# Performance work log

Measured on AMD Instinct MI355X. Metric: run time of the kernel, lower is better.

Reference implementation:

```python
import jax, jax.numpy as jnp
import numpy as np

NEG_SLOPE = 0.2   # PyG GATConv default negative_slope
BN_EPS = 1e-5


def gat_layer(x, src, dst, W, a_src, a_dst, b, num_nodes):
    """PyG-style GATConv (concat=True). src/dst already include self-loops."""
    H, C = a_src.shape
    h = (x @ W).reshape(num_nodes, H, C)            # [N,H,C]
    al_s = jnp.sum(h * a_src, axis=-1)              # [N,H] per-node src score
    al_d = jnp.sum(h * a_dst, axis=-1)              # [N,H]
    e = al_s[src] + al_d[dst]                       # [E,H]
    e = jnp.where(e > 0, e, NEG_SLOPE * e)          # leaky_relu
    m = jax.ops.segment_max(e, dst, num_segments=num_nodes)
    e = jnp.exp(e - m[dst])
    s = jax.ops.segment_sum(e, dst, num_segments=num_nodes)
    alpha = e / (s[dst] + 1e-16)                    # segment softmax over dst
    out = jax.ops.segment_sum(alpha[:, :, None] * h[src], dst, num_segments=num_nodes)
    return out.reshape(num_nodes, H * C) + b


def batch_norm(x, gamma, beta):
    mu = jnp.mean(x, axis=0)
    var = jnp.mean((x - mu) ** 2, axis=0)
    return (x - mu) * jax.lax.rsqrt(var + BN_EPS) * gamma + beta


def setup_inputs() -> dict:
    N, E, IN, H, C, L, OUT, NC = 50000, 800000, 256, 4, 64, 32, 32, 30
    HC = H * C
    key = jax.random.key(0)
    cnt = [0]
    def nk():
        cnt[0] += 1
        return jax.random.fold_in(key, cnt[0])
    def w(shape, scale):
        return jax.random.normal(nk(), shape, jnp.float32) * scale
    inp = {
        "x": jax.random.normal(nk(), (N, IN), jnp.float32),
        "edge_index": jax.random.randint(nk(), (2, E), 0, N, dtype=jnp.int32),
        "eps": jax.random.normal(nk(), (N, L), jnp.float32),
    }
    for i, d_in in zip((1, 2, 3), (IN, HC, HC)):
        inp[f"W{i}"] = w((d_in, HC), 1.0 / np.sqrt(d_in))
        inp[f"asrc{i}"] = w((H, C), 0.1)
        inp[f"adst{i}"] = w((H, C), 0.1)
        inp[f"b{i}"] = jnp.zeros((HC,), jnp.float32)
        inp[f"g{i}"] = jnp.ones((HC,), jnp.float32)
        inp[f"be{i}"] = jnp.zeros((HC,), jnp.float32)
    inp["Wr"] = w((IN, HC), 1.0 / np.sqrt(IN)); inp["br"] = jnp.zeros((HC,), jnp.float32)
    inp["Wmu"] = w((HC, L), 1.0 / np.sqrt(HC)); inp["bmu"] = jnp.zeros((L,), jnp.float32)
    inp["Wlv"] = w((HC, L), 1.0 / np.sqrt(HC)); inp["blv"] = jnp.zeros((L,), jnp.float32)
    inp["Wd"] = w((L, OUT), 1.0 / np.sqrt(L)); inp["bd"] = jnp.zeros((OUT,), jnp.float32)
    inp["Wa"] = w((HC, NC), 1.0 / np.sqrt(HC)); inp["ba"] = jnp.zeros((NC,), jnp.float32)
    return inp


def reference(x, edge_index, eps,
              W1, asrc1, adst1, b1, g1, be1,
              W2, asrc2, adst2, b2, g2, be2,
              W3, asrc3, adst3, b3, g3, be3,
              Wr, br, Wmu, bmu, Wlv, blv, Wd, bd, Wa, ba):
    N = x.shape[0]
    loop = jnp.arange(N, dtype=edge_index.dtype)   # PyG add_self_loops default
    src = jnp.concatenate([edge_index[0], loop])
    dst = jnp.concatenate([edge_index[1], loop])

    residual = x @ Wr + br                          # [N, HC]
    h = jax.nn.relu(batch_norm(gat_layer(x, src, dst, W1, asrc1, adst1, b1, N), g1, be1))
    h = jax.nn.relu(batch_norm(gat_layer(h, src, dst, W2, asrc2, adst2, b2, N), g2, be2))
    h = jax.nn.relu(batch_norm(gat_layer(h, src, dst, W3, asrc3, adst3, b3, N), g3, be3))
    enc = h + residual

    mu = enc @ Wmu + bmu
    logvar = enc @ Wlv + blv
    z = mu + eps * jnp.exp(0.5 * logvar)            # reparameterize
    out = z @ Wd + bd
    aux_out = enc @ Wa + ba
    return (out, mu, logvar, aux_out, enc)
```

## Files before the change

kernel.cpp:

```cpp
#include <hip/hip_runtime.h>
#include <cstdint>

typedef __bf16 bf16;
typedef float f32x4 __attribute__((ext_vector_type(4)));
typedef _Float16 fp16;
typedef _Float16 half8 __attribute__((ext_vector_type(8)));

#define NEG_SLOPE 0.2f
#define BN_EPS 1e-5f

__device__ __forceinline__ void gld_lds16(const void* g, void* l) {
  auto gp = reinterpret_cast<const __attribute__((address_space(1))) unsigned int*>(
      reinterpret_cast<uintptr_t>(g));
  auto lp = reinterpret_cast<__attribute__((address_space(3))) unsigned int*>(
      reinterpret_cast<uintptr_t>(l));
  __builtin_amdgcn_global_load_lds(gp, lp, 16, 0, 0);
}

__global__ __launch_bounds__(256) void k_prep(
    const float* __restrict__ Wr, const float* __restrict__ W1,
    const float* __restrict__ W2, const float* __restrict__ W3,
    fp16* __restrict__ Wt0, fp16* __restrict__ Wt1,
    fp16* __restrict__ Wt2, fp16* __restrict__ Wt3,
    const float* __restrict__ Wmu, const float* __restrict__ bmu,
    const float* __restrict__ Wlv, const float* __restrict__ blv,
    const float* __restrict__ Wa, const float* __restrict__ ba,
    fp16* __restrict__ Wh, float* __restrict__ bias_cat,
    const float* __restrict__ x, fp16* __restrict__ A16,
    int* __restrict__ counts, int N, int xb) {
  const int b = blockIdx.x, t = threadIdx.x;
  if (b < 1024) {
    const int m = b >> 8, k = b & 255;
    const float* W = (m == 0) ? Wr : (m == 1) ? W1 : (m == 2) ? W2 : W3;
    fp16* Wt = (m == 0) ? Wt0 : (m == 1) ? Wt1 : (m == 2) ? Wt2 : Wt3;
    Wt[t * 256 + k] = (fp16)W[k * 256 + t];
  } else if (b < 1280) {
    const int k = b - 1024;
    if (t < 128) {
      float v = 0.f;
      if (t < 32) v = Wmu[k * 32 + t];
      else if (t < 64) v = Wlv[k * 32 + (t - 32)];
      else if (t < 94) v = Wa[k * 30 + (t - 64)];
      Wh[t * 256 + k] = (fp16)v;
      if (k == 0) {
        float bb = 0.f;
        if (t < 32) bb = bmu[t];
        else if (t < 64) bb = blv[t - 32];
        else if (t < 94) bb = ba[t - 64];
        bias_cat[t] = bb;
      }
    }
  } else if (b < 1280 + xb) {
    const size_t base = (size_t)(b - 1280) * 1024 + t;
    const size_t total = (size_t)N * 256;
#pragma unroll
    for (int r = 0; r < 4; ++r) {
      size_t i = base + (size_t)r * 256;
      if (i < total) A16[i] = (fp16)x[i];
    }
  } else {
    const int i = (b - 1280 - xb) * 256 + t;
    if (i < N) counts[i] = 1;
  }
}

__global__ void k_count(const int* __restrict__ ei, int* counts, int E) {
  int i = blockIdx.x * 256 + threadIdx.x;
  if (i < E) atomicAdd(&counts[ei[E + i]], 1);
}

__global__ __launch_bounds__(256) void k_scan1(const int* __restrict__ counts,
                                               int* __restrict__ row_start,
                                               int* __restrict__ bsums, int N) {
  __shared__ int s[256];
  const int t = threadIdx.x;
  const int idx = blockIdx.x * 1024 + t * 4;
  int a0 = (idx + 0 < N) ? counts[idx + 0] : 0;
  int a1 = (idx + 1 < N) ? counts[idx + 1] : 0;
  int a2 = (idx + 2 < N) ? counts[idx + 2] : 0;
  int a3 = (idx + 3 < N) ? counts[idx + 3] : 0;
  const int mysum = a0 + a1 + a2 + a3;
  s[t] = mysum;
  __syncthreads();
  for (int ofs = 1; ofs < 256; ofs <<= 1) {
    int v = (t >= ofs) ? s[t - ofs] : 0;
    __syncthreads();
    s[t] += v;
    __syncthreads();
  }
  int excl = s[t] - mysum;
  if (idx + 0 < N) row_start[idx + 0] = excl;
  if (idx + 1 < N) row_start[idx + 1] = excl + a0;
  if (idx + 2 < N) row_start[idx + 2] = excl + a0 + a1;
  if (idx + 3 < N) row_start[idx + 3] = excl + a0 + a1 + a2;
  if (t == 255) bsums[blockIdx.x] = s[255];
}

__global__ void k_scan2(int* __restrict__ bsums, int* __restrict__ row_start, int nb, int N) {
  if (threadIdx.x == 0 && blockIdx.x == 0) {
    int run = 0;
    for (int i = 0; i < nb; ++i) {
      int v = bsums[i];
      bsums[i] = run;
      run += v;
    }
    row_start[N] = run;
  }
}

__global__ void k_scan3(int* __restrict__ row_start, int* __restrict__ cursor,
                        const int* __restrict__ bsums, int N) {
  int i = blockIdx.x * 256 + threadIdx.x;
  if (i < N) {
    int v = row_start[i] + bsums[i >> 10];
    row_start[i] = v;
    cursor[i] = v;
  }
}

__global__ void k_fill(const int* __restrict__ ei, int* cursor, int* __restrict__ csr_src,
                       int E, int N) {
  int i = blockIdx.x * 256 + threadIdx.x;
  if (i < E) {
    int s = ei[i], d = ei[E + i];
    int p = atomicAdd(&cursor[d], 1);
    csr_src[p] = s;
  } else if (i < E + N) {
    int n = i - E;
    int p = atomicAdd(&cursor[n], 1);
    csr_src[p] = n;
  }
}

__global__ __launch_bounds__(256) void k_gemm(
    const fp16* __restrict__ A16, const fp16* __restrict__ B16,
    const float* __restrict__ bias, float* __restrict__ Cf, fp16* __restrict__ C16,
    const float* __restrict__ asrcp, const float* __restrict__ adstp,
    float* __restrict__ alsp, float* __restrict__ aldp,
    int M, int ldc) {
  __shared__ fp16 Ash[128 * 32];
  __shared__ fp16 Bsh[128 * 32];
  const int t = threadIdx.x;
  const int wave = t >> 6, lane = t & 63;
  const int m0 = blockIdx.x * 128, n0 = blockIdx.y * 128;
  const int lrow = lane & 15, lq = lane >> 4;
  const int wm = (wave >> 1) * 64, wn = (wave & 1) * 64;

  f32x4 acc[4][4] = {};

  const int j0 = wave * 64 + lane, j1 = j0 + 256;
  const int ar0 = j0 >> 2, ar1 = j1 >> 2;
  const int ak0 = ((j0 & 3) ^ ((ar0 >> 1) & 3)) * 8;
  const int ak1 = ((j1 & 3) ^ ((ar1 >> 1) & 3)) * 8;
  const int gm0 = min(m0 + ar0, M - 1), gm1 = min(m0 + ar1, M - 1);
  const size_t oa0 = (size_t)gm0 * 256 + ak0, oa1 = (size_t)gm1 * 256 + ak1;
  const size_t ob0 = (size_t)(n0 + ar0) * 256 + ak0, ob1 = (size_t)(n0 + ar1) * 256 + ak1;
  const int l0 = wave * 512, l1 = 2048 + wave * 512;

  for (int k0 = 0; k0 < 256; k0 += 32) {
    __syncthreads();
    gld_lds16(A16 + oa0 + k0, Ash + l0);
    gld_lds16(A16 + oa1 + k0, Ash + l1);
    gld_lds16(B16 + ob0 + k0, Bsh + l0);
    gld_lds16(B16 + ob1 + k0, Bsh + l1);
    __syncthreads();
    half8 af[4], bf[4];
#pragma unroll
    for (int mi = 0; mi < 4; mi++) {
      int row = wm + mi * 16 + lrow;
      int off = row * 32 + ((lq ^ ((row >> 1) & 3)) << 3);
      af[mi] = *(const half8*)(Ash + off);
    }
#pragma unroll
    for (int ni = 0; ni < 4; ni++) {
      int row = wn + ni * 16 + lrow;
      int off = row * 32 + ((lq ^ ((row >> 1) & 3)) << 3);
      bf[ni] = *(const half8*)(Bsh + off);
    }
#pragma unroll
    for (int mi = 0; mi < 4; mi++)
#pragma unroll
      for (int ni = 0; ni < 4; ni++)
        acc[mi][ni] = __builtin_amdgcn_mfma_f32_16x16x32_f16(af[mi], bf[ni], acc[mi][ni], 0, 0, 0);
  }

#pragma unroll
  for (int mi = 0; mi < 4; mi++) {
    const int mb = m0 + wm + mi * 16 + lq * 4;
#pragma unroll
    for (int ni = 0; ni < 4; ni++) {
      const int n = n0 + wn + ni * 16 + lrow;
#pragma unroll
      for (int r = 0; r < 4; r++) {
        int m = mb + r;
        if (m < M) {
          if (C16) C16[(size_t)m * ldc + n] = (fp16)acc[mi][ni][r];
          else     Cf[(size_t)m * ldc + n] = acc[mi][ni][r] + (bias ? bias[n] : 0.f);
        }
      }
    }
  }

  if (asrcp) {
    const int headg = (n0 + wn) >> 6;
    float as4[4], ad4[4];
#pragma unroll
    for (int ni = 0; ni < 4; ni++) {
      int cg = n0 + wn + ni * 16 + lrow;
      as4[ni] = asrcp[cg];
      ad4[ni] = adstp[cg];
    }
#pragma unroll
    for (int mi = 0; mi < 4; mi++) {
      float ps[4] = {0.f, 0.f, 0.f, 0.f}, pd[4] = {0.f, 0.f, 0.f, 0.f};
#pragma unroll
      for (int ni = 0; ni < 4; ni++)
#pragma unroll
        for (int r = 0; r < 4; r++) {
          ps[r] += acc[mi][ni][r] * as4[ni];
          pd[r] += acc[mi][ni][r] * ad4[ni];
        }
#pragma unroll
      for (int o = 1; o < 16; o <<= 1)
#pragma unroll
        for (int r = 0; r < 4; r++) {
          ps[r] += __shfl_xor(ps[r], o, 64);
          pd[r] += __shfl_xor(pd[r], o, 64);
        }
      if (lrow == 0) {
#pragma unroll
        for (int r = 0; r < 4; r++) {
          int m = m0 + wm + mi * 16 + lq * 4 + r;
          if (m < M) {
            alsp[(size_t)m * 4 + headg] = ps[r];
            aldp[(size_t)m * 4 + headg] = pd[r];
          }
        }
      }
    }
  }
}

__global__ __launch_bounds__(256) void k_gather(
    const fp16* __restrict__ h16, const float* __restrict__ als, const float* __restrict__ ald,
    const int* __restrict__ row_start, const int* __restrict__ csr_src,
    const float* __restrict__ bias, fp16* __restrict__ out, float* __restrict__ stats, int N) {
  if (blockIdx.x == 0) { stats[threadIdx.x] = 0.f; stats[256 + threadIdx.x] = 0.f; }
  const int wave = threadIdx.x >> 6, lane = threadIdx.x & 63;
  const int half = lane >> 5, l32 = lane & 31;
  const int n = blockIdx.x * 8 + wave * 2 + half;
  if (n >= N) return;
  const int head = l32 >> 3;
  const int c0 = l32 * 8;
  const float adh = ald[(size_t)n * 4 + head];
  const int beg = row_start[n], end = row_start[n + 1];
  float s = 0.f;
  float acc[8] = {0.f, 0.f, 0.f, 0.f, 0.f, 0.f, 0.f, 0.f};
#pragma unroll 4
  for (int i = beg; i < end; ++i) {
    const int sidx = csr_src[i];
    float e = als[(size_t)sidx * 4 + head] + adh;
    e = e > 0.f ? e : NEG_SLOPE * e;
    const float w = __expf(e);
    s += w;
    const half8 hv = *(const half8*)(h16 + (size_t)sidx * 256 + c0);
#pragma unroll
    for (int k = 0; k < 8; ++k) acc[k] += w * (float)hv[k];
  }
  const float inv = 1.f / (s + 1e-16f);
  const float4 b1 = *(const float4*)(bias + c0);
  const float4 b2 = *(const float4*)(bias + c0 + 4);
  half8 o;
  o[0] = (fp16)(acc[0] * inv + b1.x); o[1] = (fp16)(acc[1] * inv + b1.y);
  o[2] = (fp16)(acc[2] * inv + b1.z); o[3] = (fp16)(acc[3] * inv + b1.w);
  o[4] = (fp16)(acc[4] * inv + b2.x); o[5] = (fp16)(acc[5] * inv + b2.y);
  o[6] = (fp16)(acc[6] * inv + b2.z); o[7] = (fp16)(acc[7] * inv + b2.w);
  *(half8*)(out + (size_t)n * 256 + c0) = o;
}

__global__ __launch_bounds__(256) void k_bn_stats(const fp16* __restrict__ x,
                                                  float* __restrict__ stats, int N) {
  const int t = threadIdx.x;
  int r0 = blockIdx.x * 128;
  int rend = min(r0 + 128, N);
  float s = 0.f, sq = 0.f;
  for (int r = r0; r < rend; ++r) {
    float v = (float)x[(size_t)r * 256 + t];
    s += v; sq += v * v;
  }
  atomicAdd(&stats[t], s);
  atomicAdd(&stats[256 + t], sq);
}

__global__ __launch_bounds__(256) void k_bn_apply(
    const fp16* __restrict__ x, const float* __restrict__ stats,
    const float* __restrict__ g, const float* __restrict__ be,
    fp16* __restrict__ act16, float* __restrict__ encf,
    float invN, int total) {
  int idx = blockIdx.x * 256 + threadIdx.x;
  if (idx >= total) return;
  int c = idx & 255;
  float mu = stats[c] * invN;
  float var = stats[256 + c] * invN - mu * mu;
  float v = ((float)x[idx] - mu) * rsqrtf(var + BN_EPS) * g[c] + be[c];
  v = fmaxf(v, 0.f);
  if (encf) { v += encf[idx]; encf[idx] = v; }
  act16[idx] = (fp16)v;
}

__global__ __launch_bounds__(256) void k_finish(
    const float* __restrict__ HEAD, const float* __restrict__ eps,
    const float* __restrict__ Wd, const float* __restrict__ bd,
    float* __restrict__ o_out, float* __restrict__ o_mu, float* __restrict__ o_lv,
    float* __restrict__ o_aux, int N) {
  __shared__ float sWd[1024];
  __shared__ float sZ[8][33];
  const int t = threadIdx.x;
  for (int i = t; i < 1024; i += 256) sWd[i] = Wd[i];
  __syncthreads();
  const int r = t >> 5, j = t & 31;
  const int n = blockIdx.x * 8 + r;
  if (n < N) {
    const float* hp = HEAD + (size_t)n * 128;
    float mu = hp[j];
    float lv = hp[32 + j];
    float z = mu + eps[(size_t)n * 32 + j] * __expf(0.5f * lv);
    sZ[r][j] = z;
    o_mu[(size_t)n * 32 + j] = mu;
    o_lv[(size_t)n * 32 + j] = lv;
    if (j < 30) o_aux[(size_t)n * 30 + j] = hp[64 + j];
  }
  __syncthreads();
  if (n < N) {
    float o = bd[j];
#pragma unroll
    for (int k = 0; k < 32; ++k) o += sZ[r][k] * sWd[k * 32 + j];
    o_out[(size_t)n * 32 + j] = o;
  }
}

extern "C" void kernel_launch(void* const* d_in, const int* in_sizes, int n_in,
                              void* d_out, int out_size, void* d_ws, size_t ws_size,
                              hipStream_t stream) {
  const float* x   = (const float*)d_in[0];
  const int*   ei  = (const int*)d_in[1];
  const float* eps = (const float*)d_in[2];
  const float* Wg[3]   = {(const float*)d_in[3], (const float*)d_in[9],  (const float*)d_in[15]};
  const float* asrc[3] = {(const float*)d_in[4], (const float*)d_in[10], (const float*)d_in[16]};
  const float* adst[3] = {(const float*)d_in[5], (const float*)d_in[11], (const float*)d_in[17]};
  const float* bg[3]   = {(const float*)d_in[6], (const float*)d_in[12], (const float*)d_in[18]};
  const float* gam[3]  = {(const float*)d_in[7], (const float*)d_in[13], (const float*)d_in[19]};
  const float* bet[3]  = {(const float*)d_in[8], (const float*)d_in[14], (const float*)d_in[20]};
  const float* Wr  = (const float*)d_in[21];
  const float* br  = (const float*)d_in[22];
  const float* Wmu = (const float*)d_in[23];
  const float* bmu = (const float*)d_in[24];
  const float* Wlv = (const float*)d_in[25];
  const float* blv = (const float*)d_in[26];
  const float* Wd  = (const float*)d_in[27];
  const float* bd  = (const float*)d_in[28];
  const float* Wa  = (const float*)d_in[29];
  const float* ba  = (const float*)d_in[30];

  const int N = in_sizes[0] / 256;
  const int E = in_sizes[1] / 2;

  float* outp  = (float*)d_out;
  float* o_out = outp;
  float* o_mu  = outp + (size_t)N * 32;
  float* o_lv  = outp + (size_t)N * 64;
  float* o_aux = outp + (size_t)N * 96;
  float* o_enc = outp + (size_t)N * 96 + (size_t)N * 30;

  char* p = (char*)d_ws;
  auto carve = [&](size_t bytes) -> char* {
    char* r = p;
    p += (bytes + 255) & ~(size_t)255;
    return r;
  };
  int* counts    = (int*)carve((size_t)N * 4);
  int* row_start = (int*)carve(((size_t)N + 1) * 4);
  int* cursor    = (int*)carve((size_t)N * 4);
  int* csr_src   = (int*)carve((size_t)(E + N) * 4);
  int* bsums     = (int*)carve(((size_t)N / 1024 + 2) * 4);
  fp16* Wt16[4];
  for (int i = 0; i < 4; ++i) Wt16[i] = (fp16*)carve(256 * 256 * 2);
  fp16* Wh16 = (fp16*)carve(128 * 256 * 2);
  float* bias_cat = (float*)carve(128 * 4);
  fp16* A16 = (fp16*)carve((size_t)N * 256 * 2);
  fp16* H16 = (fp16*)carve((size_t)N * 256 * 2);
  float* FHEAD = (float*)carve((size_t)N * 128 * 4);
  fp16* AGG16 = (fp16*)carve((size_t)N * 256 * 2);
  float* als = (float*)carve((size_t)N * 4 * 4);
  float* ald = (float*)carve((size_t)N * 4 * 4);
  float* stats = (float*)carve(512 * 4);

  dim3 b256(256);

  const int xb = ((int)((size_t)N * 256 + 1023)) / 1024;
  const int cb = (N + 255) / 256;
  k_prep<<<1280 + xb + cb, b256, 0, stream>>>(
      Wr, Wg[0], Wg[1], Wg[2], Wt16[0], Wt16[1], Wt16[2], Wt16[3],
      Wmu, bmu, Wlv, blv, Wa, ba, Wh16, bias_cat, x, A16, counts, N, xb);

  const int nb_scan = (N + 1023) / 1024;
  k_count<<<(E + 255) / 256, b256, 0, stream>>>(ei, counts, E);
  k_scan1<<<nb_scan, b256, 0, stream>>>(counts, row_start, bsums, N);
  k_scan2<<<1, 64, 0, stream>>>(bsums, row_start, nb_scan, N);
  k_scan3<<<(N + 255) / 256, b256, 0, stream>>>(row_start, cursor, bsums, N);
  k_fill<<<(E + N + 255) / 256, b256, 0, stream>>>(ei, cursor, csr_src, E, N);

  dim3 ggrid((N + 127) / 128, 2);
  k_gemm<<<ggrid, b256, 0, stream>>>(A16, Wt16[0], br, o_enc, nullptr,
                                     nullptr, nullptr, nullptr, nullptr, N, 256);

  const float invN = 1.0f / (float)N;
  for (int l = 0; l < 3; ++l) {
    k_gemm<<<ggrid, b256, 0, stream>>>(A16, Wt16[l + 1], nullptr, nullptr, H16,
                                       asrc[l], adst[l], als, ald, N, 256);
    k_gather<<<(N + 7) / 8, b256, 0, stream>>>(H16, als, ald, row_start, csr_src, bg[l],
                                               AGG16, stats, N);
    k_bn_stats<<<(N + 127) / 128, b256, 0, stream>>>(AGG16, stats, N);
    if (l < 2)
      k_bn_apply<<<((size_t)N * 256 + 255) / 256, b256, 0, stream>>>(
          AGG16, stats, gam[l], bet[l], A16, nullptr, invN, N * 256);
    else
      k_bn_apply<<<((size_t)N * 256 + 255) / 256, b256, 0, stream>>>(
          AGG16, stats, gam[l], bet[l], A16, o_enc, invN, N * 256);
  }

  dim3 hgrid((N + 127) / 128, 1);
  k_gemm<<<hgrid, b256, 0, stream>>>(A16, Wh16, bias_cat, FHEAD, nullptr,
                                     nullptr, nullptr, nullptr, nullptr, N, 128);
  k_finish<<<(N + 7) / 8, b256, 0, stream>>>(FHEAD, eps, Wd, bd, o_out, o_mu, o_lv, o_aux, N);
}
```

Baseline: 800.5 us.

## Fuse head GEMM with reparameterize/decoder epilogue and remap GEMM grid for XCD locality

The head projection GEMM now computes mu, logvar, z, the decoder output and aux directly in its epilogue, using shared memory for z and Wd. This removes the FHEAD intermediate buffer and the separate finish kernel. The main GEMM also switches to a 1D grid that is remapped so consecutive blocks on the same XCD share M-tiles and both N-halves of an M-tile land on the same XCD, aiming for better L2 reuse of A. The cost is extra LDS in the head kernel, and some padded blocks in the main GEMM that exit immediately.

```diff
diff --git a/kernel.cpp b/kernel.cpp
--- a/kernel.cpp
+++ b/kernel.cpp
@@ -140,9 +140,14 @@
     int M, int ldc) {
   __shared__ fp16 Ash[128 * 32];
   __shared__ fp16 Bsh[128 * 32];
+  const int nmb = (M + 127) >> 7;
+  const int b = blockIdx.x;
+  const int xcd = b & 7, q = b >> 3;
+  const int jn = q & 1, pmb = (q >> 1) * 8 + xcd;
+  if (pmb >= nmb) return;
   const int t = threadIdx.x;
   const int wave = t >> 6, lane = t & 63;
-  const int m0 = blockIdx.x * 128, n0 = blockIdx.y * 128;
+  const int m0 = pmb * 128, n0 = jn * 128;
   const int lrow = lane & 15, lq = lane >> 4;
   const int wm = (wave >> 1) * 64, wn = (wave & 1) * 64;
 
@@ -237,6 +242,116 @@
           }
         }
       }
+    }
+  }
+}
+
+__global__ __launch_bounds__(256) void k_gemm_head(
+    const fp16* __restrict__ A16, const fp16* __restrict__ B16,
+    const float* __restrict__ bias_cat, const float* __restrict__ eps,
+    const float* __restrict__ Wd, const float* __restrict__ bd,
+    float* __restrict__ o_out, float* __restrict__ o_mu, float* __restrict__ o_lv,
+    float* __restrict__ o_aux, int M) {
+  __shared__ fp16 Ash[128 * 32];
+  __shared__ fp16 Bsh[128 * 32];
+  __shared__ float sZ[128][33];
+  __shared__ float sWd[1024];
+  const int t = threadIdx.x;
+  const int wave = t >> 6, lane = t & 63;
+  const int m0 = blockIdx.x * 128;
+  const int lrow = lane & 15, lq = lane >> 4;
+  const int wm = (wave >> 1) * 64, wn = (wave & 1) * 64;
+
+  f32x4 acc[4][4] = {};
+
+  const int j0 = wave * 64 + lane, j1 = j0 + 256;
+  const int ar0 = j0 >> 2, ar1 = j1 >> 2;
+  const int ak0 = ((j0 & 3) ^ ((ar0 >> 1) & 3)) * 8;
+  const int ak1 = ((j1 & 3) ^ ((ar1 >> 1) & 3)) * 8;
+  const int gm0 = min(m0 + ar0, M - 1), gm1 = min(m0 + ar1, M - 1);
+  const size_t oa0 = (size_t)gm0 * 256 + ak0, oa1 = (size_t)gm1 * 256 + ak1;
+  const size_t ob0 = (size_t)ar0 * 256 + ak0, ob1 = (size_t)ar1 * 256 + ak1;
+  const int l0 = wave * 512, l1 = 2048 + wave * 512;
+
+  for (int k0 = 0; k0 < 256; k0 += 32) {
+    __syncthreads();
+    gld_lds16(A16 + oa0 + k0, Ash + l0);
+    gld_lds16(A16 + oa1 + k0, Ash + l1);
+    gld_lds16(B16 + ob0 + k0, Bsh + l0);
+    gld_lds16(B16 + ob1 + k0, Bsh + l1);
+    __syncthreads();
+    half8 af[4], bf[4];
+#pragma unroll
+    for (int mi = 0; mi < 4; mi++) {
+      int row = wm + mi * 16 + lrow;
+      int off = row * 32 + ((lq ^ ((row >> 1) & 3)) << 3);
+      af[mi] = *(const half8*)(Ash + off);
+    }
+#pragma unroll
+    for (int ni = 0; ni < 4; ni++) {
+      int row = wn + ni * 16 + lrow;
+      int off = row * 32 + ((lq ^ ((row >> 1) & 3)) << 3);
+      bf[ni] = *(const half8*)(Bsh + off);
+    }
+#pragma unroll
+    for (int mi = 0; mi < 4; mi++)
+#pragma unroll
+      for (int ni = 0; ni < 4; ni++)
+        acc[mi][ni] = __builtin_amdgcn_mfma_f32_16x16x32_f16(af[mi], bf[ni], acc[mi][ni], 0, 0, 0);
+  }
+
+  for (int i = t; i < 1024; i += 256) sWd[i] = Wd[i];
+
+  if ((wave & 1) == 0) {
+#pragma unroll
+    for (int mi = 0; mi < 4; mi++) {
+      const int lrb = wm + mi * 16 + lq * 4;
+      const int mb = m0 + lrb;
+#pragma unroll
+      for (int ni = 0; ni < 2; ni++) {
+        const int jj = ni * 16 + lrow;
+#pragma unroll
+        for (int r = 0; r < 4; r++) {
+          const int m = mb + r;
+          if (m < M) {
+            float mu = acc[mi][ni][r] + bias_cat[jj];
+            float lv = acc[mi][ni + 2][r] + bias_cat[32 + jj];
+            float z = mu + eps[(size_t)m * 32 + jj] * __expf(0.5f * lv);
+            o_mu[(size_t)m * 32 + jj] = mu;
+            o_lv[(size_t)m * 32 + jj] = lv;
+            sZ[lrb + r][jj] = z;
+          }
+        }
+      }
+    }
+  } else {
+#pragma unroll
+    for (int mi = 0; mi < 4; mi++) {
+      const int mb = m0 + wm + mi * 16 + lq * 4;
+#pragma unroll
+      for (int ni = 0; ni < 4; ni++) {
+        const int n = 64 + ni * 16 + lrow;
+        if (n < 94) {
+#pragma unroll
+          for (int r = 0; r < 4; r++) {
+            const int m = mb + r;
+            if (m < M) o_aux[(size_t)m * 30 + (n - 64)] = acc[mi][ni][r] + bias_cat[n];
+          }
+        }
+      }
+    }
+  }
+  __syncthreads();
+  const int jc = t & 31, rr = t >> 5;
+#pragma unroll
+  for (int it = 0; it < 16; ++it) {
+    const int lr = it * 8 + rr;
+    const int m = m0 + lr;
+    if (m < M) {
+      float o = bd[jc];
+#pragma unroll
+      for (int k = 0; k < 32; ++k) o += sZ[lr][k] * sWd[k * 32 + jc];
+      o_out[(size_t)m * 32 + jc] = o;
     }
   }
 }
@@ -308,37 +423,6 @@
   act16[idx] = (fp16)v;
 }
 
-__global__ __launch_bounds__(256) void k_finish(
-    const float* __restrict__ HEAD, const float* __restrict__ eps,
-    const float* __restrict__ Wd, const float* __restrict__ bd,
-    float* __restrict__ o_out, float* __restrict__ o_mu, float* __restrict__ o_lv,
-    float* __restrict__ o_aux, int N) {
-  __shared__ float sWd[1024];
-  __shared__ float sZ[8][33];
-  const int t = threadIdx.x;
-  for (int i = t; i < 1024; i += 256) sWd[i] = Wd[i];
-  __syncthreads();
-  const int r = t >> 5, j = t & 31;
-  const int n = blockIdx.x * 8 + r;
-  if (n < N) {
-    const float* hp = HEAD + (size_t)n * 128;
-    float mu = hp[j];
-    float lv = hp[32 + j];
-    float z = mu + eps[(size_t)n * 32 + j] * __expf(0.5f * lv);
-    sZ[r][j] = z;
-    o_mu[(size_t)n * 32 + j] = mu;
-    o_lv[(size_t)n * 32 + j] = lv;
-    if (j < 30) o_aux[(size_t)n * 30 + j] = hp[64 + j];
-  }
-  __syncthreads();
-  if (n < N) {
-    float o = bd[j];
-#pragma unroll
-    for (int k = 0; k < 32; ++k) o += sZ[r][k] * sWd[k * 32 + j];
-    o_out[(size_t)n * 32 + j] = o;
-  }
-}
-
 extern "C" void kernel_launch(void* const* d_in, const int* in_sizes, int n_in,
                               void* d_out, int out_size, void* d_ws, size_t ws_size,
                               hipStream_t stream) {
@@ -389,7 +473,6 @@
   float* bias_cat = (float*)carve(128 * 4);
   fp16* A16 = (fp16*)carve((size_t)N * 256 * 2);
   fp16* H16 = (fp16*)carve((size_t)N * 256 * 2);
-  float* FHEAD = (float*)carve((size_t)N * 128 * 4);
   fp16* AGG16 = (fp16*)carve((size_t)N * 256 * 2);
   float* als = (float*)carve((size_t)N * 4 * 4);
   float* ald = (float*)carve((size_t)N * 4 * 4);
@@ -410,14 +493,15 @@
   k_scan3<<<(N + 255) / 256, b256, 0, stream>>>(row_start, cursor, bsums, N);
   k_fill<<<(E + N + 255) / 256, b256, 0, stream>>>(ei, cursor, csr_src, E, N);
 
-  dim3 ggrid((N + 127) / 128, 2);
-  k_gemm<<<ggrid, b256, 0, stream>>>(A16, Wt16[0], br, o_enc, nullptr,
-                                     nullptr, nullptr, nullptr, nullptr, N, 256);
+  const int nmb = (N + 127) / 128;
+  const int g1d = 8 * ((nmb + 7) / 8) * 2;
+  k_gemm<<<g1d, b256, 0, stream>>>(A16, Wt16[0], br, o_enc, nullptr,
+                                   nullptr, nullptr, nullptr, nullptr, N, 256);
 
   const float invN = 1.0f / (float)N;
   for (int l = 0; l < 3; ++l) {
-    k_gemm<<<ggrid, b256, 0, stream>>>(A16, Wt16[l + 1], nullptr, nullptr, H16,
-                                       asrc[l], adst[l], als, ald, N, 256);
+    k_gemm<<<g1d, b256, 0, stream>>>(A16, Wt16[l + 1], nullptr, nullptr, H16,
+                                     asrc[l], adst[l], als, ald, N, 256);
     k_gather<<<(N + 7) / 8, b256, 0, stream>>>(H16, als, ald, row_start, csr_src, bg[l],
                                                AGG16, stats, N);
     k_bn_stats<<<(N + 127) / 128, b256, 0, stream>>>(AGG16, stats, N);
@@ -429,8 +513,6 @@
           AGG16, stats, gam[l], bet[l], A16, o_enc, invN, N * 256);
   }
 
-  dim3 hgrid((N + 127) / 128, 1);
-  k_gemm<<<hgrid, b256, 0, stream>>>(A16, Wh16, bias_cat, FHEAD, nullptr,
-                                     nullptr, nullptr, nullptr, nullptr, N, 128);
-  k_finish<<<(N + 7) / 8, b256, 0, stream>>>(FHEAD, eps, Wd, bd, o_out, o_mu, o_lv, o_aux, N);
-}
+  k_gemm_head<<<nmb, b256, 0, stream>>>(A16, Wh16, bias_cat, eps, Wd, bd,
+                                        o_out, o_mu, o_lv, o_aux, N);
+}
```

Result: no change. 787.5 us (-1.6%).
